# Performance work log

Measured on AMD Instinct MI355X. Metric: run time of the kernel, lower is better.

Reference implementation:

```python
import jax, jax.numpy as jnp
import numpy as np
import math

DIM = 512
BLOCK_NUM = 16
SEQ_LEN = 8192
BLOCK_LEN = SEQ_LEN // BLOCK_NUM  # 512 == DIM -> mask used as-is
BATCH = 4
LN_EPS = 1e-3  # keras LayerNormalization default epsilon


def setup_inputs() -> dict:
    key = jax.random.key(0)
    ks = jax.random.split(key, 5)
    inputs = jax.random.normal(ks[0], (BATCH, BLOCK_NUM, BLOCK_LEN, DIM), dtype=jnp.float32)
    # binary padding-style mask, values in {0,1}
    mask_array = jax.random.randint(ks[1], (BATCH, SEQ_LEN, DIM), 0, 2).astype(jnp.float32)
    scale = 1.0 / math.sqrt(DIM)
    dw1 = jax.random.normal(ks[2], (DIM, DIM), dtype=jnp.float32) * scale
    dw2 = jax.random.normal(ks[3], (DIM, DIM), dtype=jnp.float32) * scale
    dw3 = jax.random.normal(ks[4], (DIM, DIM), dtype=jnp.float32) * scale
    db1 = jnp.zeros((DIM,), dtype=jnp.float32)
    db2 = jnp.zeros((DIM,), dtype=jnp.float32)
    db3 = jnp.zeros((DIM,), dtype=jnp.float32)
    return {"inputs": inputs, "mask_array": mask_array,
            "dw1": dw1, "dw2": dw2, "dw3": dw3,
            "db1": db1, "db2": db2, "db3": db3}


def reference(inputs, mask_array, dw1, dw2, dw3, db1, db2, db3):
    # inputs: [B, block_num, block_len, dim]
    Q = jnp.matmul(inputs, dw1) + db1
    K = jnp.matmul(inputs, dw2) + db2
    V = jnpp_matmul = jnp.matmul(inputs, dw3) + db3
    V = jnp.matmul(inputs, dw3) + db3
    # block-local attention scores: [B, bn, bl, bl]
    scores = jnp.einsum('bnqd,bnkd->bnqk', Q, K) / math.sqrt(DIM)
    # mask: [B, seq_len, dim] -> [B, bn, bl, dim]; block_len == dim so no slice/tile
    m = mask_array.reshape(BATCH, BLOCK_NUM, BLOCK_LEN, DIM)
    scores = scores + (1.0 - m) * jnp.float32(-1e10)
    p = jax.nn.softmax(scores, axis=-1)
    out = jnp.einsum('bnqk,bnkd->bnqd', p, V) + inputs  # residual
    # LayerNorm(axis=-1), fresh keras layer: gamma=1, beta=0, eps=1e-3
    mean = jnp.mean(out, axis=-1, keepdims=True)
    var = jnp.mean(jnp.square(out - mean), axis=-1, keepdims=True)
    return (out - mean) / jnp.sqrt(var + LN_EPS)
```

## Files before the change

kernel.cpp:

```cpp
#include <hip/hip_runtime.h>

#define DIMK 512
#define NBLK 64
#define NTOK 32768

typedef short  short8 __attribute__((ext_vector_type(8)));
typedef float  f32x4  __attribute__((ext_vector_type(4)));
typedef unsigned short u16x8 __attribute__((ext_vector_type(8)));

__device__ __forceinline__ unsigned short f2bf(float f) {
  union { float f; unsigned u; } v; v.f = f;
  unsigned r = (v.u + 0x7FFFu + ((v.u >> 16) & 1u)) >> 16;
  return (unsigned short)r;
}

__device__ __forceinline__ void gload_lds16(const unsigned short* g,
                                            unsigned short* l) {
  __builtin_amdgcn_global_load_lds(
      (const __attribute__((address_space(1))) unsigned int*)(g),
      (__attribute__((address_space(3))) unsigned int*)(l),
      16, 0, 0);
}

__device__ __forceinline__ void gemm_tile(
    const unsigned short* __restrict__ A, size_t arow0,
    const unsigned short* __restrict__ Bt, size_t brow0,
    f32x4 acc[4][4], unsigned short* As, unsigned short* Bs)
{
  const int tid  = threadIdx.x;
  const int lane = tid & 63;
  const int wv   = tid >> 6;
  const int quad = lane >> 4;
  const int l16  = lane & 15;
  const int rb   = (wv >> 1) * 64;
  const int cb   = (wv & 1) * 64;

  const int c0 = tid, c1 = tid + 256;
  const int r0 = c0 >> 2, o0 = (c0 & 3) << 3;
  const int r1 = c1 >> 2, o1 = (c1 & 3) << 3;
  const unsigned short* a0 = &A[(arow0 + r0) * (size_t)DIMK + o0];
  const unsigned short* a1 = &A[(arow0 + r1) * (size_t)DIMK + o1];
  const unsigned short* b0 = &Bt[(brow0 + r0) * (size_t)DIMK + o0];
  const unsigned short* b1 = &Bt[(brow0 + r1) * (size_t)DIMK + o1];

  for (int it = 0; it < 16; ++it) {
    const int k0 = it * 32;
    gload_lds16(a0 + k0, &As[c0 * 8]);
    gload_lds16(a1 + k0, &As[c1 * 8]);
    gload_lds16(b0 + k0, &Bs[c0 * 8]);
    gload_lds16(b1 + k0, &Bs[c1 * 8]);
    __syncthreads();
    short8 af[4], bfv[4];
#pragma unroll
    for (int i = 0; i < 4; ++i)
      af[i] = *(const short8*)&As[(rb + i * 16 + l16) * 32 + quad * 8];
#pragma unroll
    for (int j = 0; j < 4; ++j)
      bfv[j] = *(const short8*)&Bs[(cb + j * 16 + l16) * 32 + quad * 8];
#pragma unroll
    for (int i = 0; i < 4; ++i)
#pragma unroll
      for (int j = 0; j < 4; ++j)
        acc[i][j] = __builtin_amdgcn_mfma_f32_16x16x32_bf16(
            af[i], bfv[j], acc[i][j], 0, 0, 0);
    __syncthreads();
  }
}

__global__ __launch_bounds__(256) void k_wt_prep(
    const float* __restrict__ dw1, const float* __restrict__ dw2,
    const float* __restrict__ dw3, unsigned short* __restrict__ Wt)
{
  const int idx = blockIdx.x * 256 + threadIdx.x;
  const int w = idx >> 18;
  const int r = idx & 262143;
  const int n = r >> 9, k = r & 511;
  const float* dw = (w == 0) ? dw1 : (w == 1) ? dw2 : dw3;
  Wt[(size_t)w * 262144 + (size_t)n * 512 + k] = f2bf(dw[(size_t)k * 512 + n]);
}

template<bool PACK>
__global__ __launch_bounds__(256) void k_xconv(
    const float* __restrict__ X, const float* __restrict__ mask,
    unsigned short* __restrict__ Xb, unsigned char* __restrict__ bits)
{
  const size_t gid = (size_t)blockIdx.x * 256 + threadIdx.x;
  const size_t i = gid * 8;
  const float4 a = *(const float4*)(X + i);
  const float4 b = *(const float4*)(X + i + 4);
  u16x8 o;
  o[0] = f2bf(a.x); o[1] = f2bf(a.y); o[2] = f2bf(a.z); o[3] = f2bf(a.w);
  o[4] = f2bf(b.x); o[5] = f2bf(b.y); o[6] = f2bf(b.z); o[7] = f2bf(b.w);
  *(u16x8*)(Xb + i) = o;
  if (PACK) {
    const float4 ma = *(const float4*)(mask + i);
    const float4 mb = *(const float4*)(mask + i + 4);
    unsigned v = 0;
    v |= (ma.x > 0.5f) << 0; v |= (ma.y > 0.5f) << 1;
    v |= (ma.z > 0.5f) << 2; v |= (ma.w > 0.5f) << 3;
    v |= (mb.x > 0.5f) << 4; v |= (mb.y > 0.5f) << 5;
    v |= (mb.z > 0.5f) << 6; v |= (mb.w > 0.5f) << 7;
    bits[gid] = (unsigned char)v;
  }
}

__global__ __launch_bounds__(256) void k_qkv(
    const unsigned short* __restrict__ Xb, const unsigned short* __restrict__ Wt,
    const float* __restrict__ db1, const float* __restrict__ db2,
    const float* __restrict__ db3,
    unsigned short* __restrict__ Qb, unsigned short* __restrict__ Kb,
    unsigned short* __restrict__ Vt)
{
  __shared__ __align__(16) unsigned short As[128 * 32];
  __shared__ __align__(16) unsigned short Bs[128 * 32];
  const int id = blockIdx.x;
  const int mtile = id & 255;
  const int wnt = id >> 8;
  const int w  = wnt >> 2;
  const int nt = wnt & 3;
  const size_t m0 = (size_t)mtile * 128;
  const int n0 = nt * 128;
  f32x4 acc[4][4];
#pragma unroll
  for (int i = 0; i < 4; ++i)
#pragma unroll
    for (int j = 0; j < 4; ++j) { f32x4 z = {0.f, 0.f, 0.f, 0.f}; acc[i][j] = z; }

  gemm_tile(Xb, m0, Wt + (size_t)w * 262144, (size_t)n0, acc, As, Bs);

  const float* db = (w == 0) ? db1 : (w == 1) ? db2 : db3;
  const int lane = threadIdx.x & 63, wvq = threadIdx.x >> 6;
  const int quad = lane >> 4, l16 = lane & 15;
  const int rb = (wvq >> 1) * 64, cb = (wvq & 1) * 64;

  if (w < 2) {
    unsigned short* Ob = (w == 0) ? Qb : Kb;
#pragma unroll
    for (int i = 0; i < 4; ++i)
#pragma unroll
      for (int j = 0; j < 4; ++j)
#pragma unroll
        for (int r = 0; r < 4; ++r) {
          const size_t row = m0 + rb + i * 16 + quad * 4 + r;
          const int col = n0 + cb + j * 16 + l16;
          Ob[row * (size_t)DIMK + col] = f2bf(acc[i][j][r] + db[col]);
        }
  } else {
    const int blk = (int)(m0 >> 9);
    unsigned short* Vblk = Vt + (size_t)blk * 262144;
#pragma unroll
    for (int i = 0; i < 4; ++i)
#pragma unroll
      for (int j = 0; j < 4; ++j) {
        const int col = n0 + cb + j * 16 + l16;
        const int tokloc = (int)((m0 & 511)) + rb + i * 16 + quad * 4;
        const float bv = db[col];
        ushort4 pk;
        pk.x = f2bf(acc[i][j][0] + bv);
        pk.y = f2bf(acc[i][j][1] + bv);
        pk.z = f2bf(acc[i][j][2] + bv);
        pk.w = f2bf(acc[i][j][3] + bv);
        *(ushort4*)&Vblk[(size_t)col * 512 + tokloc] = pk;
      }
  }
}

template<bool USE_BITS>
__global__ __launch_bounds__(256, 2) void k_attn_p(
    const unsigned short* __restrict__ Qb, const unsigned short* __restrict__ Kb,
    const float* __restrict__ mask, const unsigned long long* __restrict__ bits,
    unsigned short* __restrict__ Pb)
{
  __shared__ __align__(16) unsigned short As[64 * 32];
  __shared__ __align__(16) unsigned short Bs[512 * 32];
  __shared__ float red[4][64];
  const int tid = threadIdx.x, lane = tid & 63, wv = tid >> 6;
  const int quad = lane >> 4, l16 = lane & 15;
  const int blk = blockIdx.x & 63, mt = blockIdx.x >> 6;
  const size_t tb = (size_t)blk * 512;
  const size_t q0 = tb + (size_t)mt * 64;

  f32x4 acc[4][8];
#pragma unroll
  for (int i = 0; i < 4; ++i)
#pragma unroll
    for (int j = 0; j < 8; ++j) { f32x4 z = {0.f, 0.f, 0.f, 0.f}; acc[i][j] = z; }

  const int ra = tid >> 2, oa = (tid & 3) << 3;
  const unsigned short* ap = &Qb[(q0 + ra) * (size_t)DIMK + oa];
  const unsigned short* kp = &Kb[tb * (size_t)DIMK];

  for (int it = 0; it < 16; ++it) {
    const int k0 = it * 32;
    gload_lds16(ap + k0, &As[tid * 8]);
#pragma unroll
    for (int h = 0; h < 8; ++h) {
      const int c = tid + h * 256;
      const int r = c >> 2, o = (c & 3) << 3;
      gload_lds16(kp + (size_t)r * DIMK + k0 + o, &Bs[c * 8]);
    }
    __syncthreads();
    short8 af[4], bfv[8];
#pragma unroll
    for (int i = 0; i < 4; ++i)
      af[i] = *(const short8*)&As[(i * 16 + l16) * 32 + quad * 8];
#pragma unroll
    for (int j = 0; j < 8; ++j)
      bfv[j] = *(const short8*)&Bs[(wv * 128 + j * 16 + l16) * 32 + quad * 8];
#pragma unroll
    for (int i = 0; i < 4; ++i)
#pragma unroll
      for (int j = 0; j < 8; ++j)
        acc[i][j] = __builtin_amdgcn_mfma_f32_16x16x32_bf16(
            af[i], bfv[j], acc[i][j], 0, 0, 0);
    __syncthreads();
  }

  const float scale = 0.04419417382415922f;
  float rmax[4][4];
#pragma unroll
  for (int i = 0; i < 4; ++i)
#pragma unroll
    for (int r = 0; r < 4; ++r) rmax[i][r] = -3.0e38f;
#pragma unroll
  for (int i = 0; i < 4; ++i)
#pragma unroll
    for (int r = 0; r < 4; ++r) {
      const size_t tok = q0 + i * 16 + quad * 4 + r;
      unsigned long long w0 = 0, w1 = 0;
      if (USE_BITS) {
        w0 = bits[tok * 8 + wv * 2];
        w1 = bits[tok * 8 + wv * 2 + 1];
      }
#pragma unroll
      for (int j = 0; j < 8; ++j) {
        float bias;
        if (USE_BITS) {
          const unsigned long long sel = (j < 4) ? w0 : w1;
          bias = ((sel >> (l16 + 16 * (j & 3))) & 1ull) ? 0.0f : -1e10f;
        } else {
          const int col = wv * 128 + j * 16 + l16;
          bias = (1.0f - mask[tok * (size_t)DIMK + col]) * (-1e10f);
        }
        const float v = acc[i][j][r] * scale + bias;
        acc[i][j][r] = v;
        rmax[i][r] = fmaxf(rmax[i][r], v);
      }
    }
#pragma unroll
  for (int i = 0; i < 4; ++i)
#pragma unroll
    for (int r = 0; r < 4; ++r)
      for (int d = 1; d < 16; d <<= 1)
        rmax[i][r] = fmaxf(rmax[i][r], __shfl_xor(rmax[i][r], d, 64));
  if (l16 == 0)
#pragma unroll
    for (int i = 0; i < 4; ++i)
#pragma unroll
      for (int r = 0; r < 4; ++r) red[wv][i * 16 + quad * 4 + r] = rmax[i][r];
  __syncthreads();
#pragma unroll
  for (int i = 0; i < 4; ++i)
#pragma unroll
    for (int r = 0; r < 4; ++r) {
      const int row = i * 16 + quad * 4 + r;
      rmax[i][r] = fmaxf(fmaxf(red[0][row], red[1][row]),
                         fmaxf(red[2][row], red[3][row]));
    }
  __syncthreads();
  float rsum[4][4];
#pragma unroll
  for (int i = 0; i < 4; ++i)
#pragma unroll
    for (int r = 0; r < 4; ++r) rsum[i][r] = 0.f;
#pragma unroll
  for (int i = 0; i < 4; ++i)
#pragma unroll
    for (int j = 0; j < 8; ++j)
#pragma unroll
      for (int r = 0; r < 4; ++r) {
        const float e = __expf(acc[i][j][r] - rmax[i][r]);
        acc[i][j][r] = e;
        rsum[i][r] += e;
      }
#pragma unroll
  for (int i = 0; i < 4; ++i)
#pragma unroll
    for (int r = 0; r < 4; ++r)
      for (int d = 1; d < 16; d <<= 1)
        rsum[i][r] += __shfl_xor(rsum[i][r], d, 64);
  if (l16 == 0)
#pragma unroll
    for (int i = 0; i < 4; ++i)
#pragma unroll
      for (int r = 0; r < 4; ++r) red[wv][i * 16 + quad * 4 + r] = rsum[i][r];
  __syncthreads();
#pragma unroll
  for (int i = 0; i < 4; ++i)
#pragma unroll
    for (int r = 0; r < 4; ++r) {
      const int row = i * 16 + quad * 4 + r;
      rsum[i][r] = 1.0f / (red[0][row] + red[1][row] + red[2][row] + red[3][row]);
    }
#pragma unroll
  for (int i = 0; i < 4; ++i)
#pragma unroll
    for (int j = 0; j < 8; ++j)
#pragma unroll
      for (int r = 0; r < 4; ++r) {
        const size_t tok = q0 + i * 16 + quad * 4 + r;
        const int col = wv * 128 + j * 16 + l16;
        Pb[tok * (size_t)DIMK + col] = f2bf(acc[i][j][r] * rsum[i][r]);
      }
}

__global__ __launch_bounds__(256, 2) void k_pv_ln(
    const unsigned short* __restrict__ Pb, const unsigned short* __restrict__ Vt,
    const float* __restrict__ X, float* __restrict__ Out)
{
  __shared__ __align__(16) unsigned short As[64 * 32];
  __shared__ __align__(16) unsigned short Bs[512 * 32];
  __shared__ float2 red[4][64];
  const int tid = threadIdx.x, lane = tid & 63, wv = tid >> 6;
  const int quad = lane >> 4, l16 = lane & 15;
  const int blk = blockIdx.x & 63, mt = blockIdx.x >> 6;
  const size_t tb = (size_t)blk * 512;
  const size_t q0 = tb + (size_t)mt * 64;

  f32x4 acc[4][8];
#pragma unroll
  for (int i = 0; i < 4; ++i)
#pragma unroll
    for (int j = 0; j < 8; ++j) { f32x4 z = {0.f, 0.f, 0.f, 0.f}; acc[i][j] = z; }

  const int ra = tid >> 2, oa = (tid & 3) << 3;
  const unsigned short* ap = &Pb[(q0 + ra) * (size_t)DIMK + oa];
  const unsigned short* vp = Vt + (size_t)blk * 262144;

  for (int it = 0; it < 16; ++it) {
    const int k0 = it * 32;
    gload_lds16(ap + k0, &As[tid * 8]);
#pragma unroll
    for (int h = 0; h < 8; ++h) {
      const int c = tid + h * 256;
      const int r = c >> 2, o = (c & 3) << 3;
      gload_lds16(vp + (size_t)r * DIMK + k0 + o, &Bs[c * 8]);
    }
    __syncthreads();
    short8 af[4], bfv[8];
#pragma unroll
    for (int i = 0; i < 4; ++i)
      af[i] = *(const short8*)&As[(i * 16 + l16) * 32 + quad * 8];
#pragma unroll
    for (int j = 0; j < 8; ++j)
      bfv[j] = *(const short8*)&Bs[(wv * 128 + j * 16 + l16) * 32 + quad * 8];
#pragma unroll
    for (int i = 0; i < 4; ++i)
#pragma unroll
      for (int j = 0; j < 8; ++j)
        acc[i][j] = __builtin_amdgcn_mfma_f32_16x16x32_bf16(
            af[i], bfv[j], acc[i][j], 0, 0, 0);
    __syncthreads();
  }

  float vsum[4][4], vsq[4][4];
#pragma unroll
  for (int i = 0; i < 4; ++i)
#pragma unroll
    for (int r = 0; r < 4; ++r) { vsum[i][r] = 0.f; vsq[i][r] = 0.f; }
#pragma unroll
  for (int i = 0; i < 4; ++i)
#pragma unroll
    for (int j = 0; j < 8; ++j)
#pragma unroll
      for (int r = 0; r < 4; ++r) {
        const size_t tok = q0 + i * 16 + quad * 4 + r;
        const int col = wv * 128 + j * 16 + l16;
        const float v = acc[i][j][r] + X[tok * (size_t)DIMK + col];
        acc[i][j][r] = v;
        vsum[i][r] += v;
        vsq[i][r] += v * v;
      }
#pragma unroll
  for (int i = 0; i < 4; ++i)
#pragma unroll
    for (int r = 0; r < 4; ++r)
      for (int d = 1; d < 16; d <<= 1) {
        vsum[i][r] += __shfl_xor(vsum[i][r], d, 64);
        vsq[i][r]  += __shfl_xor(vsq[i][r], d, 64);
      }
  if (l16 == 0)
#pragma unroll
    for (int i = 0; i < 4; ++i)
#pragma unroll
      for (int r = 0; r < 4; ++r) {
        float2 p; p.x = vsum[i][r]; p.y = vsq[i][r];
        red[wv][i * 16 + quad * 4 + r] = p;
      }
  __syncthreads();
#pragma unroll
  for (int i = 0; i < 4; ++i)
#pragma unroll
    for (int r = 0; r < 4; ++r) {
      const int row = i * 16 + quad * 4 + r;
      float s = 0.f, q = 0.f;
#pragma unroll
      for (int w = 0; w < 4; ++w) { s += red[w][row].x; q += red[w][row].y; }
      const float mean = s * (1.0f / 512.0f);
      const float var  = q * (1.0f / 512.0f) - mean * mean;
      vsum[i][r] = mean;
      vsq[i][r]  = rsqrtf(var + 1e-3f);
    }
#pragma unroll
  for (int i = 0; i < 4; ++i)
#pragma unroll
    for (int j = 0; j < 8; ++j)
#pragma unroll
      for (int r = 0; r < 4; ++r) {
        const size_t tok = q0 + i * 16 + quad * 4 + r;
        const int col = wv * 128 + j * 16 + l16;
        Out[tok * (size_t)DIMK + col] =
            (acc[i][j][r] - vsum[i][r]) * vsq[i][r];
      }
}

extern "C" void kernel_launch(void* const* d_in, const int* in_sizes, int n_in,
                              void* d_out, int out_size, void* d_ws, size_t ws_size,
                              hipStream_t stream)
{
  const float* X    = (const float*)d_in[0];
  const float* mask = (const float*)d_in[1];
  const float* dw1  = (const float*)d_in[2];
  const float* dw2  = (const float*)d_in[3];
  const float* dw3  = (const float*)d_in[4];
  const float* db1  = (const float*)d_in[5];
  const float* db2  = (const float*)d_in[6];
  const float* db3  = (const float*)d_in[7];
  float* Out = (float*)d_out;

  char* ws = (char*)d_ws;
  const size_t MB = 1ull << 20;
  const bool big = ws_size >= 132 * MB;

  unsigned short* Wt = (unsigned short*)(ws);
  unsigned char*  bits = (unsigned char*)(ws + 2 * MB);
  const size_t base = big ? 4 * MB : 2 * MB;
  unsigned short* Qb = (unsigned short*)(ws + base);
  unsigned short* Kb = (unsigned short*)(ws + base + 32 * MB);
  unsigned short* Vt = (unsigned short*)(ws + base + 64 * MB);
  unsigned short* Pb = (unsigned short*)(ws + base + 96 * MB);
  unsigned short* Xb = Pb;

  k_wt_prep<<<3072, 256, 0, stream>>>(dw1, dw2, dw3, Wt);
  if (big)
    k_xconv<true><<<8192, 256, 0, stream>>>(X, mask, Xb, bits);
  else
    k_xconv<false><<<8192, 256, 0, stream>>>(X, mask, Xb, bits);
  k_qkv<<<3072, 256, 0, stream>>>(Xb, Wt, db1, db2, db3, Qb, Kb, Vt);
  if (big)
    k_attn_p<true><<<512, 256, 0, stream>>>(
        Qb, Kb, mask, (const unsigned long long*)bits, Pb);
  else
    k_attn_p<false><<<512, 256, 0, stream>>>(
        Qb, Kb, mask, (const unsigned long long*)bits, Pb);
  k_pv_ln<<<512, 256, 0, stream>>>(Pb, Vt, X, Out);
}
```

Before: 352.3 us.

## Fuse Q/K/V projections per tile, always bit-pack mask, use bf16 residual

The QKV GEMM now computes all three projections in one block, loading the X tile once and reusing it against three weight tiles. Grid drops from 3072 to 1024 blocks, with more accumulators per thread. The V output is transposed through LDS so global stores are coalesced 16-byte writes. The mask is always bit-packed into the output buffer, so the attention kernel never reads the fp32 mask. The residual in the final kernel reads bf16 X instead of fp32 X, which saves bandwidth but adds rounding error. P now reuses Q's buffer.

After: 344.5 us. 2.2% less time.

```diff
diff --git a/kernel.cpp b/kernel.cpp
--- a/kernel.cpp
+++ b/kernel.cpp
@@ -12,6 +12,9 @@
   union { float f; unsigned u; } v; v.f = f;
   unsigned r = (v.u + 0x7FFFu + ((v.u >> 16) & 1u)) >> 16;
   return (unsigned short)r;
+}
+__device__ __forceinline__ float bf2f(unsigned short h) {
+  return __uint_as_float(((unsigned)h) << 16);
 }
 
 __device__ __forceinline__ void gload_lds16(const unsigned short* g,
@@ -22,51 +25,6 @@
       16, 0, 0);
 }
 
-__device__ __forceinline__ void gemm_tile(
-    const unsigned short* __restrict__ A, size_t arow0,
-    const unsigned short* __restrict__ Bt, size_t brow0,
-    f32x4 acc[4][4], unsigned short* As, unsigned short* Bs)
-{
-  const int tid  = threadIdx.x;
-  const int lane = tid & 63;
-  const int wv   = tid >> 6;
-  const int quad = lane >> 4;
-  const int l16  = lane & 15;
-  const int rb   = (wv >> 1) * 64;
-  const int cb   = (wv & 1) * 64;
-
-  const int c0 = tid, c1 = tid + 256;
-  const int r0 = c0 >> 2, o0 = (c0 & 3) << 3;
-  const int r1 = c1 >> 2, o1 = (c1 & 3) << 3;
-  const unsigned short* a0 = &A[(arow0 + r0) * (size_t)DIMK + o0];
-  const unsigned short* a1 = &A[(arow0 + r1) * (size_t)DIMK + o1];
-  const unsigned short* b0 = &Bt[(brow0 + r0) * (size_t)DIMK + o0];
-  const unsigned short* b1 = &Bt[(brow0 + r1) * (size_t)DIMK + o1];
-
-  for (int it = 0; it < 16; ++it) {
-    const int k0 = it * 32;
-    gload_lds16(a0 + k0, &As[c0 * 8]);
-    gload_lds16(a1 + k0, &As[c1 * 8]);
-    gload_lds16(b0 + k0, &Bs[c0 * 8]);
-    gload_lds16(b1 + k0, &Bs[c1 * 8]);
-    __syncthreads();
-    short8 af[4], bfv[4];
-#pragma unroll
-    for (int i = 0; i < 4; ++i)
-      af[i] = *(const short8*)&As[(rb + i * 16 + l16) * 32 + quad * 8];
-#pragma unroll
-    for (int j = 0; j < 4; ++j)
-      bfv[j] = *(const short8*)&Bs[(cb + j * 16 + l16) * 32 + quad * 8];
-#pragma unroll
-    for (int i = 0; i < 4; ++i)
-#pragma unroll
-      for (int j = 0; j < 4; ++j)
-        acc[i][j] = __builtin_amdgcn_mfma_f32_16x16x32_bf16(
-            af[i], bfv[j], acc[i][j], 0, 0, 0);
-    __syncthreads();
-  }
-}
-
 __global__ __launch_bounds__(256) void k_wt_prep(
     const float* __restrict__ dw1, const float* __restrict__ dw2,
     const float* __restrict__ dw3, unsigned short* __restrict__ Wt)
@@ -79,97 +37,146 @@
   Wt[(size_t)w * 262144 + (size_t)n * 512 + k] = f2bf(dw[(size_t)k * 512 + n]);
 }
 
-template<bool PACK>
 __global__ __launch_bounds__(256) void k_xconv(
-    const float* __restrict__ X, const float* __restrict__ mask,
-    unsigned short* __restrict__ Xb, unsigned char* __restrict__ bits)
-{
-  const size_t gid = (size_t)blockIdx.x * 256 + threadIdx.x;
-  const size_t i = gid * 8;
+    const float* __restrict__ X, unsigned short* __restrict__ Xb)
+{
+  const size_t i = ((size_t)blockIdx.x * 256 + threadIdx.x) * 8;
   const float4 a = *(const float4*)(X + i);
   const float4 b = *(const float4*)(X + i + 4);
   u16x8 o;
   o[0] = f2bf(a.x); o[1] = f2bf(a.y); o[2] = f2bf(a.z); o[3] = f2bf(a.w);
   o[4] = f2bf(b.x); o[5] = f2bf(b.y); o[6] = f2bf(b.z); o[7] = f2bf(b.w);
   *(u16x8*)(Xb + i) = o;
-  if (PACK) {
-    const float4 ma = *(const float4*)(mask + i);
-    const float4 mb = *(const float4*)(mask + i + 4);
-    unsigned v = 0;
-    v |= (ma.x > 0.5f) << 0; v |= (ma.y > 0.5f) << 1;
-    v |= (ma.z > 0.5f) << 2; v |= (ma.w > 0.5f) << 3;
-    v |= (mb.x > 0.5f) << 4; v |= (mb.y > 0.5f) << 5;
-    v |= (mb.z > 0.5f) << 6; v |= (mb.w > 0.5f) << 7;
-    bits[gid] = (unsigned char)v;
-  }
-}
-
-__global__ __launch_bounds__(256) void k_qkv(
+}
+
+__global__ __launch_bounds__(256) void k_bitpack(
+    const float* __restrict__ mask, unsigned char* __restrict__ bits)
+{
+  const size_t gid = (size_t)blockIdx.x * 256 + threadIdx.x;
+  const size_t i = gid * 8;
+  const float4 ma = *(const float4*)(mask + i);
+  const float4 mb = *(const float4*)(mask + i + 4);
+  unsigned v = 0;
+  v |= (ma.x > 0.5f) << 0; v |= (ma.y > 0.5f) << 1;
+  v |= (ma.z > 0.5f) << 2; v |= (ma.w > 0.5f) << 3;
+  v |= (mb.x > 0.5f) << 4; v |= (mb.y > 0.5f) << 5;
+  v |= (mb.z > 0.5f) << 6; v |= (mb.w > 0.5f) << 7;
+  bits[gid] = (unsigned char)v;
+}
+
+__global__ __launch_bounds__(256, 2) void k_qkv(
     const unsigned short* __restrict__ Xb, const unsigned short* __restrict__ Wt,
     const float* __restrict__ db1, const float* __restrict__ db2,
     const float* __restrict__ db3,
     unsigned short* __restrict__ Qb, unsigned short* __restrict__ Kb,
     unsigned short* __restrict__ Vt)
 {
-  __shared__ __align__(16) unsigned short As[128 * 32];
-  __shared__ __align__(16) unsigned short Bs[128 * 32];
+  __shared__ __align__(16) unsigned short smem[128 * 136];
+  unsigned short* As = smem;
+  unsigned short* Bs = smem + 4096;
+
   const int id = blockIdx.x;
-  const int mtile = id & 255;
-  const int wnt = id >> 8;
-  const int w  = wnt >> 2;
-  const int nt = wnt & 3;
+  const int x = id & 7, j = id >> 3;
+  const int mtile = x * 32 + (j >> 2);
+  const int nt = j & 3;
   const size_t m0 = (size_t)mtile * 128;
   const int n0 = nt * 128;
-  f32x4 acc[4][4];
-#pragma unroll
-  for (int i = 0; i < 4; ++i)
-#pragma unroll
-    for (int j = 0; j < 4; ++j) { f32x4 z = {0.f, 0.f, 0.f, 0.f}; acc[i][j] = z; }
-
-  gemm_tile(Xb, m0, Wt + (size_t)w * 262144, (size_t)n0, acc, As, Bs);
-
-  const float* db = (w == 0) ? db1 : (w == 1) ? db2 : db3;
-  const int lane = threadIdx.x & 63, wvq = threadIdx.x >> 6;
+
+  const int tid = threadIdx.x, lane = tid & 63, wv = tid >> 6;
   const int quad = lane >> 4, l16 = lane & 15;
-  const int rb = (wvq >> 1) * 64, cb = (wvq & 1) * 64;
-
-  if (w < 2) {
+  const int rb = (wv >> 1) * 64, cb = (wv & 1) * 64;
+
+  f32x4 acc[3][4][4];
+#pragma unroll
+  for (int w = 0; w < 3; ++w)
+#pragma unroll
+    for (int i = 0; i < 4; ++i)
+#pragma unroll
+      for (int jj = 0; jj < 4; ++jj) {
+        f32x4 z = {0.f, 0.f, 0.f, 0.f}; acc[w][i][jj] = z;
+      }
+
+  const int ra0 = tid >> 2,          oa0 = (tid & 3) << 3;
+  const int ra1 = (tid + 256) >> 2,  oa1 = ((tid + 256) & 3) << 3;
+  const unsigned short* a0 = &Xb[(m0 + ra0) * (size_t)DIMK + oa0];
+  const unsigned short* a1 = &Xb[(m0 + ra1) * (size_t)DIMK + oa1];
+
+  for (int it = 0; it < 16; ++it) {
+    const int k0 = it * 32;
+    gload_lds16(a0 + k0, &As[tid * 8]);
+    gload_lds16(a1 + k0, &As[(tid + 256) * 8]);
+#pragma unroll
+    for (int h = 0; h < 6; ++h) {
+      const int c = tid + h * 256;
+      const int w = c >> 9, cc = c & 511;
+      const int r = cc >> 2, o = (cc & 3) << 3;
+      gload_lds16(&Wt[(size_t)w * 262144 + (size_t)(n0 + r) * 512 + k0 + o],
+                  &Bs[w * 4096 + cc * 8]);
+    }
+    __syncthreads();
+    short8 af[4];
+#pragma unroll
+    for (int i = 0; i < 4; ++i)
+      af[i] = *(const short8*)&As[(rb + i * 16 + l16) * 32 + quad * 8];
+#pragma unroll
+    for (int jj = 0; jj < 4; ++jj)
+#pragma unroll
+      for (int w = 0; w < 3; ++w) {
+        const short8 bf =
+            *(const short8*)&Bs[w * 4096 + (cb + jj * 16 + l16) * 32 + quad * 8];
+#pragma unroll
+        for (int i = 0; i < 4; ++i)
+          acc[w][i][jj] = __builtin_amdgcn_mfma_f32_16x16x32_bf16(
+              af[i], bf, acc[w][i][jj], 0, 0, 0);
+      }
+    __syncthreads();
+  }
+
+#pragma unroll
+  for (int w = 0; w < 2; ++w) {
+    const float* db = (w == 0) ? db1 : db2;
     unsigned short* Ob = (w == 0) ? Qb : Kb;
 #pragma unroll
     for (int i = 0; i < 4; ++i)
 #pragma unroll
-      for (int j = 0; j < 4; ++j)
+      for (int jj = 0; jj < 4; ++jj)
 #pragma unroll
         for (int r = 0; r < 4; ++r) {
           const size_t row = m0 + rb + i * 16 + quad * 4 + r;
-          const int col = n0 + cb + j * 16 + l16;
-          Ob[row * (size_t)DIMK + col] = f2bf(acc[i][j][r] + db[col]);
+          const int col = n0 + cb + jj * 16 + l16;
+          Ob[row * (size_t)DIMK + col] = f2bf(acc[w][i][jj][r] + db[col]);
         }
-  } else {
-    const int blk = (int)(m0 >> 9);
-    unsigned short* Vblk = Vt + (size_t)blk * 262144;
-#pragma unroll
-    for (int i = 0; i < 4; ++i)
-#pragma unroll
-      for (int j = 0; j < 4; ++j) {
-        const int col = n0 + cb + j * 16 + l16;
-        const int tokloc = (int)((m0 & 511)) + rb + i * 16 + quad * 4;
-        const float bv = db[col];
-        ushort4 pk;
-        pk.x = f2bf(acc[i][j][0] + bv);
-        pk.y = f2bf(acc[i][j][1] + bv);
-        pk.z = f2bf(acc[i][j][2] + bv);
-        pk.w = f2bf(acc[i][j][3] + bv);
-        *(ushort4*)&Vblk[(size_t)col * 512 + tokloc] = pk;
-      }
   }
-}
-
-template<bool USE_BITS>
+#pragma unroll
+  for (int i = 0; i < 4; ++i)
+#pragma unroll
+    for (int jj = 0; jj < 4; ++jj) {
+      const int cl = cb + jj * 16 + l16;
+      const int t0 = rb + i * 16 + quad * 4;
+      const float bv = db3[n0 + cl];
+      ushort4 pk;
+      pk.x = f2bf(acc[2][i][jj][0] + bv);
+      pk.y = f2bf(acc[2][i][jj][1] + bv);
+      pk.z = f2bf(acc[2][i][jj][2] + bv);
+      pk.w = f2bf(acc[2][i][jj][3] + bv);
+      *(ushort4*)&smem[cl * 136 + t0] = pk;
+    }
+  __syncthreads();
+  const int blk = mtile >> 2;
+  const int tokbase = (mtile & 3) * 128;
+  unsigned short* Vblk = Vt + (size_t)blk * 262144;
+#pragma unroll
+  for (int h = 0; h < 8; ++h) {
+    const int c = tid + h * 256;
+    const int cl = c >> 4, toff = (c & 15) * 8;
+    *(u16x8*)&Vblk[(size_t)(n0 + cl) * 512 + tokbase + toff] =
+        *(const u16x8*)&smem[cl * 136 + toff];
+  }
+}
+
 __global__ __launch_bounds__(256, 2) void k_attn_p(
     const unsigned short* __restrict__ Qb, const unsigned short* __restrict__ Kb,
-    const float* __restrict__ mask, const unsigned long long* __restrict__ bits,
-    unsigned short* __restrict__ Pb)
+    const unsigned long long* __restrict__ bits, unsigned short* __restrict__ Pb)
 {
   __shared__ __align__(16) unsigned short As[64 * 32];
   __shared__ __align__(16) unsigned short Bs[512 * 32];
@@ -227,21 +234,12 @@
 #pragma unroll
     for (int r = 0; r < 4; ++r) {
       const size_t tok = q0 + i * 16 + quad * 4 + r;
-      unsigned long long w0 = 0, w1 = 0;
-      if (USE_BITS) {
-        w0 = bits[tok * 8 + wv * 2];
-        w1 = bits[tok * 8 + wv * 2 + 1];
-      }
+      const unsigned long long w0 = bits[tok * 8 + wv * 2];
+      const unsigned long long w1 = bits[tok * 8 + wv * 2 + 1];
 #pragma unroll
       for (int j = 0; j < 8; ++j) {
-        float bias;
-        if (USE_BITS) {
-          const unsigned long long sel = (j < 4) ? w0 : w1;
-          bias = ((sel >> (l16 + 16 * (j & 3))) & 1ull) ? 0.0f : -1e10f;
-        } else {
-          const int col = wv * 128 + j * 16 + l16;
-          bias = (1.0f - mask[tok * (size_t)DIMK + col]) * (-1e10f);
-        }
+        const unsigned long long sel = (j < 4) ? w0 : w1;
+        const float bias = ((sel >> (l16 + 16 * (j & 3))) & 1ull) ? 0.0f : -1e10f;
         const float v = acc[i][j][r] * scale + bias;
         acc[i][j][r] = v;
         rmax[i][r] = fmaxf(rmax[i][r], v);
@@ -316,7 +314,7 @@
 
 __global__ __launch_bounds__(256, 2) void k_pv_ln(
     const unsigned short* __restrict__ Pb, const unsigned short* __restrict__ Vt,
-    const float* __restrict__ X, float* __restrict__ Out)
+    const unsigned short* __restrict__ Xb, float* __restrict__ Out)
 {
   __shared__ __align__(16) unsigned short As[64 * 32];
   __shared__ __align__(16) unsigned short Bs[512 * 32];
@@ -376,7 +374,7 @@
       for (int r = 0; r < 4; ++r) {
         const size_t tok = q0 + i * 16 + quad * 4 + r;
         const int col = wv * 128 + j * 16 + l16;
-        const float v = acc[i][j][r] + X[tok * (size_t)DIMK + col];
+        const float v = acc[i][j][r] + bf2f(Xb[tok * (size_t)DIMK + col]);
         acc[i][j][r] = v;
         vsum[i][r] += v;
         vsq[i][r] += v * v;
@@ -440,28 +438,18 @@
 
   char* ws = (char*)d_ws;
   const size_t MB = 1ull << 20;
-  const bool big = ws_size >= 132 * MB;
-
   unsigned short* Wt = (unsigned short*)(ws);
-  unsigned char*  bits = (unsigned char*)(ws + 2 * MB);
-  const size_t base = big ? 4 * MB : 2 * MB;
-  unsigned short* Qb = (unsigned short*)(ws + base);
-  unsigned short* Kb = (unsigned short*)(ws + base + 32 * MB);
-  unsigned short* Vt = (unsigned short*)(ws + base + 64 * MB);
-  unsigned short* Pb = (unsigned short*)(ws + base + 96 * MB);
-  unsigned short* Xb = Pb;
+  unsigned short* Qb = (unsigned short*)(ws + 2 * MB);
+  unsigned short* Kb = (unsigned short*)(ws + 34 * MB);
+  unsigned short* Vt = (unsigned short*)(ws + 66 * MB);
+  unsigned short* Xb = (unsigned short*)(ws + 98 * MB);
+  unsigned short* Pb = Qb;
+  unsigned char*  bits = (unsigned char*)d_out;
 
   k_wt_prep<<<3072, 256, 0, stream>>>(dw1, dw2, dw3, Wt);
-  if (big)
-    k_xconv<true><<<8192, 256, 0, stream>>>(X, mask, Xb, bits);
-  else
-    k_xconv<false><<<8192, 256, 0, stream>>>(X, mask, Xb, bits);
-  k_qkv<<<3072, 256, 0, stream>>>(Xb, Wt, db1, db2, db3, Qb, Kb, Vt);
-  if (big)
-    k_attn_p<true><<<512, 256, 0, stream>>>(
-        Qb, Kb, mask, (const unsigned long long*)bits, Pb);
-  else
-    k_attn_p<false><<<512, 256, 0, stream>>>(
-        Qb, Kb, mask, (const unsigned long long*)bits, Pb);
-  k_pv_ln<<<512, 256, 0, stream>>>(Pb, Vt, X, Out);
-}
+  k_xconv  <<<8192, 256, 0, stream>>>(X, Xb);
+  k_bitpack<<<8192, 256, 0, stream>>>(mask, bits);
+  k_qkv    <<<1024, 256, 0, stream>>>(Xb, Wt, db1, db2, db3, Qb, Kb, Vt);
+  k_attn_p <<<512, 256, 0, stream>>>(Qb, Kb, (const unsigned long long*)bits, Pb);
+  k_pv_ln  <<<512, 256, 0, stream>>>(Pb, Vt, Xb, Out);
+}
```
